# Optimization experiments

Measured on AMD Instinct MI355X. Metric: run time of the kernel, lower is better.

## Reference

```python
import jax, jax.numpy as jnp
import numpy as np
from jax import lax


def _conv(x, w, b, pad):
    # x: [B,C,H,W], w: [O,I,kh,kw]
    y = lax.conv_general_dilated(x, w, (1, 1), [(pad, pad), (pad, pad)],
                                 dimension_numbers=('NCHW', 'OIHW', 'NCHW'))
    return y + b[None, :, None, None]


def _maxpool2(x):
    return lax.reduce_window(x, -jnp.inf, lax.max, (1, 1, 2, 2), (1, 1, 2, 2), 'VALID')


def setup_inputs() -> dict:
    key = jax.random.key(0)
    ks = jax.random.split(key, 6)
    N, T, R, D = 8, 64, 9, 512
    x = jax.random.normal(ks[0], (N, T, R, D), dtype=jnp.float32)
    x = x / jnp.linalg.norm(x, axis=-1, keepdims=True)  # ViSiL features are L2-normalized
    w1 = jax.random.normal(ks[1], (32, 1, 3, 3), dtype=jnp.float32) * 0.05
    w2 = jax.random.normal(ks[2], (64, 32, 3, 3), dtype=jnp.float32) * 0.05
    w3 = jax.random.normal(ks[3], (128, 64, 3, 3), dtype=jnp.float32) * 0.05
    w4 = jax.random.normal(ks[4], (1, 128, 1, 1), dtype=jnp.float32) * 0.05
    return {
        'x': x,
        'w1': w1, 'b1': jnp.zeros((32,), jnp.float32),
        'w2': w2, 'b2': jnp.zeros((64,), jnp.float32),
        'w3': w3, 'b3': jnp.zeros((128,), jnp.float32),
        'w4': w4, 'b4': jnp.zeros((1,), jnp.float32),
    }


def reference(x, w1, b1, w2, b2, w3, b3, w4, b4):
    N, T, R, D = x.shape
    # frame-to-frame similarity: region correlation volume + chamfer (max over p, mean over o)
    sim = jnp.einsum('aiok,bjpk->aiopjb', x, x)        # [a,i,o,p,j,b]
    sim = jnp.mean(jnp.max(sim, axis=3), axis=2)        # [a,i,j,b]
    sim = jnp.transpose(sim, (0, 3, 1, 2)).reshape(N * N, 1, T, T)  # '(a b) () i j'
    # VideoComparator CNN head (ZeroPad2d(1) + valid 3x3 conv == 'same' 3x3 conv)
    h = jax.nn.relu(_conv(sim, w1, b1, 1))
    h = _maxpool2(h)
    h = jax.nn.relu(_conv(h, w2, b2, 1))
    h = _maxpool2(h)
    h = jax.nn.relu(_conv(h, w3, b3, 1))
    h = _conv(h, w4, b4, 0)                              # [N*N, 1, T/4, T/4]
    # SimilarityRegularizationLoss(min_val=-1, max_val=1)
    loss = jnp.sum(jax.nn.relu(-(h + 1.0))) + jnp.sum(jax.nn.relu(h - 1.0))
    # Hardtanh, rescale to [0,1], then video-to-video chamfer
    s = jnp.clip(h, -1.0, 1.0) / 2.0 + 0.5
    s = jnp.mean(jnp.max(s, axis=3), axis=2)             # [N*N, 1]
    return s.reshape(N, N), loss
```

## Files before the change

### kernel.cpp

```cpp
#include <hip/hip_runtime.h>

typedef unsigned short u16;
typedef unsigned int u32;
typedef __bf16 bf16x8 __attribute__((ext_vector_type(8)));
typedef u16 u16x8 __attribute__((ext_vector_type(8)));
typedef float f32x4 __attribute__((ext_vector_type(4)));

__device__ __forceinline__ u16 f2bf(float f) {
  u32 u = __float_as_uint(f);
  u32 r = (u + 0x7FFFu + ((u >> 16) & 1u)) >> 16;
  return (u16)r;
}

__device__ __forceinline__ void gload16(const void* g, void* l) {
  typedef __attribute__((address_space(1))) const void gvoid;
  typedef __attribute__((address_space(3))) void lvoid;
  __builtin_amdgcn_global_load_lds((gvoid*)g, (lvoid*)l, 16, 0, 0);
}

__global__ void k_cast(const float* __restrict__ x, u16* __restrict__ A) {
  int t = blockIdx.x * 256 + threadIdx.x;
  const float4* xp = (const float4*)x + (size_t)t * 2;
  float4 v0 = xp[0], v1 = xp[1];
  u16x8 r;
  r[0] = f2bf(v0.x); r[1] = f2bf(v0.y); r[2] = f2bf(v0.z); r[3] = f2bf(v0.w);
  r[4] = f2bf(v1.x); r[5] = f2bf(v1.y); r[6] = f2bf(v1.z); r[7] = f2bf(v1.w);
  *(u16x8*)(A + (size_t)t * 8) = r;
}

__global__ __launch_bounds__(256) void k_gemm_smax(const u16* __restrict__ A,
                                                   float* __restrict__ Smax) {
  __shared__ char smem[53248];
  u16* As = (u16*)smem;
  u16* Bs = (u16*)(smem + 16384);
  const int rb = blockIdx.x, cb = blockIdx.y;
  const int rowBase = rb * 128, colBase = cb * 288;
  const int tid = threadIdx.x, wave = tid >> 6, lane = tid & 63;
  const int lr = lane >> 3, lc = lane & 7;
  const int lrow = lane & 15, lk = lane >> 4;
  const int xr = lrow & 7;
  const int wr = (wave & 1) * 64, wc = (wave >> 1) * 144;

  f32x4 acc[4][9];
#pragma unroll
  for (int rt = 0; rt < 4; ++rt)
#pragma unroll
    for (int ct = 0; ct < 9; ++ct) { f32x4 z = {0.f, 0.f, 0.f, 0.f}; acc[rt][ct] = z; }

  for (int k0 = 0; k0 < 512; k0 += 64) {
    __syncthreads();
#pragma unroll
    for (int ii = 0; ii < 4; ++ii) {
      int r0 = wave * 32 + ii * 8;
      gload16(A + (size_t)(rowBase + r0 + lr) * 512 + k0 + ((lc ^ lr) * 8),
              As + r0 * 64);
    }
#pragma unroll
    for (int jj = 0; jj < 9; ++jj) {
      int c0 = wave * 72 + jj * 8;
      gload16(A + (size_t)(colBase + c0 + lr) * 512 + k0 + ((lc ^ lr) * 8),
              Bs + c0 * 64);
    }
    __syncthreads();
#pragma unroll
    for (int s = 0; s < 2; ++s) {
      bf16x8 af[4], bf[9];
#pragma unroll
      for (int rt = 0; rt < 4; ++rt)
        af[rt] = *(const bf16x8*)(As + (wr + rt * 16 + lrow) * 64 +
                                  ((u32)(s * 4 + lk) ^ xr) * 8);
#pragma unroll
      for (int ct = 0; ct < 9; ++ct)
        bf[ct] = *(const bf16x8*)(Bs + (wc + ct * 16 + lrow) * 64 +
                                  ((u32)(s * 4 + lk) ^ xr) * 8);
#pragma unroll
      for (int rt = 0; rt < 4; ++rt)
#pragma unroll
        for (int ct = 0; ct < 9; ++ct)
          acc[rt][ct] = __builtin_amdgcn_mfma_f32_16x16x32_bf16(af[rt], bf[ct],
                                                                acc[rt][ct], 0, 0, 0);
    }
  }

  float* epi = (float*)smem + wave * 2368;
  const int w2 = wave >> 1;
#pragma unroll
  for (int rt = 0; rt < 4; ++rt) {
    __syncthreads();
#pragma unroll
    for (int ct = 0; ct < 9; ++ct)
#pragma unroll
      for (int r = 0; r < 4; ++r)
        epi[(lk * 4 + r) * 148 + ct * 16 + lrow] = acc[rt][ct][r];
    __syncthreads();
#pragma unroll
    for (int q = 0; q < 4; ++q) {
      int o = lane + 64 * q;
      int row = o >> 4, g = o & 15;
      const float* p = epi + row * 148 + g * 9;
      float m = p[0];
#pragma unroll
      for (int t = 1; t < 9; ++t) m = fmaxf(m, p[t]);
      Smax[(size_t)(rowBase + wr + rt * 16 + row) * 512 + cb * 32 + w2 * 16 + g] = m;
    }
  }
}

__global__ void k_reduce_o(const float* __restrict__ Smax, float* __restrict__ sim) {
  int idx = blockIdx.x * 256 + threadIdx.x;
  int j = idx & 63, i = (idx >> 6) & 63, b = (idx >> 12) & 7, a = idx >> 15;
  const float* p = Smax + (size_t)((a * 64 + i) * 9) * 512 + b * 64 + j;
  float s = p[0];
#pragma unroll
  for (int o = 1; o < 9; ++o) s += p[o * 512];
  sim[idx] = s * (1.f / 9.f);
}

__global__ void k_wpack(const float* __restrict__ w2, const float* __restrict__ w3,
                        u16* __restrict__ p2, u16* __restrict__ p3) {
  int i = blockIdx.x * 256 + threadIdx.x;
  if (i < 18432) {
    int t = i >> 11, oc = (i >> 5) & 63, ic = i & 31;
    p2[i] = f2bf(w2[(oc * 32 + ic) * 9 + t]);
  }
  {
    int t = i >> 13, oc = (i >> 6) & 127, ic = i & 63;
    p3[i] = f2bf(w3[(oc * 64 + ic) * 9 + t]);
  }
}

__global__ __launch_bounds__(256) void k_conv1pool(const float* __restrict__ sim,
                                                   const float* __restrict__ w1,
                                                   const float* __restrict__ b1,
                                                   u16* __restrict__ h1) {
  __shared__ float tin[4096];
  const int pair = blockIdx.x, ocg = blockIdx.y, tid = threadIdx.x;
  const float4* src = (const float4*)(sim + (size_t)pair * 4096);
  for (int i = tid; i < 1024; i += 256) ((float4*)tin)[i] = src[i];
  __syncthreads();
  float wv[8][9], bs[8];
#pragma unroll
  for (int o = 0; o < 8; ++o) {
#pragma unroll
    for (int q = 0; q < 9; ++q) wv[o][q] = w1[(ocg * 8 + o) * 9 + q];
    bs[o] = b1[ocg * 8 + o];
  }
  for (int pp = tid; pp < 1024; pp += 256) {
    int py = pp >> 5, px = pp & 31;
    float m[8];
#pragma unroll
    for (int o = 0; o < 8; ++o) m[o] = 0.f;
#pragma unroll
    for (int dy = 0; dy < 2; ++dy)
#pragma unroll
      for (int dx = 0; dx < 2; ++dx) {
        float s[8];
#pragma unroll
        for (int o = 0; o < 8; ++o) s[o] = bs[o];
        int yy = py * 2 + dy, xx0 = px * 2 + dx;
#pragma unroll
        for (int ky = 0; ky < 3; ++ky) {
          int y = yy + ky - 1;
          if ((unsigned)y < 64u) {
#pragma unroll
            for (int kx = 0; kx < 3; ++kx) {
              int x = xx0 + kx - 1;
              if ((unsigned)x < 64u) {
                float v = tin[y * 64 + x];
#pragma unroll
                for (int o = 0; o < 8; ++o) s[o] += wv[o][ky * 3 + kx] * v;
              }
            }
          }
        }
#pragma unroll
        for (int o = 0; o < 8; ++o) m[o] = fmaxf(m[o], fmaxf(s[o], 0.f));
      }
    u16x8 r;
#pragma unroll
    for (int o = 0; o < 8; ++o) r[o] = f2bf(m[o]);
    *(u16x8*)&h1[(((size_t)pair * 32 + py) * 32 + px) * 32 + ocg * 8] = r;
  }
}

__global__ __launch_bounds__(256) void k_conv2pool(const u16* __restrict__ h1,
                                                   const u16* __restrict__ wp2,
                                                   const float* __restrict__ b2,
                                                   u16* __restrict__ h2) {
  __shared__ u16 tile[18 * 34 * 40];
  const int pair = blockIdx.x, yh = blockIdx.y, tid = threadIdx.x;
  const int wave = tid >> 6, lane = tid & 63, l15 = lane & 15, quad = lane >> 4;
  u16x8 z8 = {0, 0, 0, 0, 0, 0, 0, 0};
  for (int i = tid; i < 3060; i += 256) ((u16x8*)tile)[i] = z8;
  __syncthreads();
  for (int f = tid; f < 1152; f += 256) {
    int i = f >> 6, rem = f & 63, px = rem >> 1, half = rem & 1;
    int gr = yh * 16 - 1 + i;
    if ((unsigned)gr < 32u)
      *(u16x8*)&tile[(i * 34 + 1 + px) * 40 + half * 16] =
          *(const u16x8*)&h1[(((size_t)pair * 32 + gr) * 32 + px) * 32 + half * 16];
  }
  __syncthreads();

  f32x4 acc[8][4];
#pragma unroll
  for (int m = 0; m < 8; ++m)
#pragma unroll
    for (int n = 0; n < 4; ++n) { f32x4 z = {0.f, 0.f, 0.f, 0.f}; acc[m][n] = z; }

  for (int t = 0; t < 9; ++t) {
    int ky = t / 3, kx = t % 3;
    bf16x8 wf[4];
#pragma unroll
    for (int nt = 0; nt < 4; ++nt)
      wf[nt] = *(const bf16x8*)&wp2[((t * 64 + nt * 16 + l15) << 5) + quad * 8];
#pragma unroll
    for (int rr = 0; rr < 4; ++rr)
#pragma unroll
      for (int xh = 0; xh < 2; ++xh) {
        int lr = wave * 4 + rr;
        bf16x8 af = *(const bf16x8*)&tile[((lr + ky) * 34 + xh * 16 + l15 + kx) * 40 +
                                          quad * 8];
#pragma unroll
        for (int nt = 0; nt < 4; ++nt)
          acc[rr * 2 + xh][nt] =
              __builtin_amdgcn_mfma_f32_16x16x32_bf16(af, wf[nt], acc[rr * 2 + xh][nt],
                                                      0, 0, 0);
      }
  }

  float bv[4];
#pragma unroll
  for (int nt = 0; nt < 4; ++nt) bv[nt] = b2[nt * 16 + l15];
#pragma unroll
  for (int rp = 0; rp < 2; ++rp)
#pragma unroll
    for (int xh = 0; xh < 2; ++xh) {
      int py = yh * 8 + wave * 2 + rp;
      int px0 = xh * 8 + quad * 2;
#pragma unroll
      for (int nt = 0; nt < 4; ++nt) {
        f32x4 va = acc[(rp * 2) * 2 + xh][nt], vb = acc[(rp * 2 + 1) * 2 + xh][nt];
        float p0 = fmaxf(fmaxf(fmaxf(va[0], va[1]), fmaxf(vb[0], vb[1])) + bv[nt], 0.f);
        float p1 = fmaxf(fmaxf(fmaxf(va[2], va[3]), fmaxf(vb[2], vb[3])) + bv[nt], 0.f);
        size_t base = (((size_t)pair * 16 + py) * 16 + px0) * 64 + nt * 16 + l15;
        h2[base] = f2bf(p0);
        h2[base + 64] = f2bf(p1);
      }
    }
}

__global__ __launch_bounds__(256) void k_conv3(const u16* __restrict__ h2,
                                               const u16* __restrict__ wp3,
                                               const float* __restrict__ b3,
                                               float* __restrict__ h3) {
  __shared__ u16 tile[18 * 18 * 72];
  const int pair = blockIdx.x, oh = blockIdx.y, tid = threadIdx.x;
  const int wave = tid >> 6, lane = tid & 63, l15 = lane & 15, quad = lane >> 4;
  u16x8 z8 = {0, 0, 0, 0, 0, 0, 0, 0};
  for (int i = tid; i < 2916; i += 256) ((u16x8*)tile)[i] = z8;
  __syncthreads();
  for (int f = tid; f < 2048; f += 256) {
    int row = f >> 7, rem = f & 127, px = rem >> 3, seg = rem & 7;
    *(u16x8*)&tile[((row + 1) * 18 + px + 1) * 72 + seg * 8] =
        *(const u16x8*)&h2[(((size_t)pair * 16 + row) * 16 + px) * 64 + seg * 8];
  }
  __syncthreads();

  f32x4 acc[4][4];
#pragma unroll
  for (int m = 0; m < 4; ++m)
#pragma unroll
    for (int n = 0; n < 4; ++n) { f32x4 z = {0.f, 0.f, 0.f, 0.f}; acc[m][n] = z; }

  for (int t = 0; t < 9; ++t) {
    int ky = t / 3, kx = t % 3;
#pragma unroll
    for (int s = 0; s < 2; ++s) {
      bf16x8 wf[4];
#pragma unroll
      for (int nt = 0; nt < 4; ++nt)
        wf[nt] = *(const bf16x8*)&wp3[((t * 128 + oh * 64 + nt * 16 + l15) << 6) +
                                      s * 32 + quad * 8];
#pragma unroll
      for (int yt = 0; yt < 4; ++yt) {
        int y = wave * 4 + yt;
        bf16x8 af = *(const bf16x8*)&tile[((y + ky) * 18 + l15 + kx) * 72 + s * 32 +
                                          quad * 8];
#pragma unroll
        for (int nt = 0; nt < 4; ++nt)
          acc[yt][nt] = __builtin_amdgcn_mfma_f32_16x16x32_bf16(af, wf[nt],
                                                                acc[yt][nt], 0, 0, 0);
      }
    }
  }

  float bv[4];
#pragma unroll
  for (int nt = 0; nt < 4; ++nt) bv[nt] = b3[oh * 64 + nt * 16 + l15];
#pragma unroll
  for (int yt = 0; yt < 4; ++yt)
#pragma unroll
    for (int nt = 0; nt < 4; ++nt)
#pragma unroll
      for (int r = 0; r < 4; ++r) {
        int px = (wave * 4 + yt) * 16 + quad * 4 + r;
        h3[((size_t)pair * 256 + px) * 128 + oh * 64 + nt * 16 + l15] =
            fmaxf(acc[yt][nt][r] + bv[nt], 0.f);
      }
}

__global__ void k_zero(float* __restrict__ out) {
  if (threadIdx.x < 65) out[threadIdx.x] = 0.f;
}

__global__ __launch_bounds__(256) void k_conv4(const float* __restrict__ h3,
                                               const float* __restrict__ w4,
                                               const float* __restrict__ b4,
                                               float* __restrict__ out) {
  __shared__ float ws4[128];
  __shared__ float rowmax[16];
  __shared__ float lsum[4];
  const int pair = blockIdx.x, tid = threadIdx.x;
  if (tid < 128) ws4[tid] = w4[tid];
  __syncthreads();
  float h = b4[0];
  const float4* p = (const float4*)(h3 + ((size_t)pair * 256 + tid) * 128);
#pragma unroll 8
  for (int i = 0; i < 32; ++i) {
    float4 v = p[i];
    h += v.x * ws4[i * 4] + v.y * ws4[i * 4 + 1] + v.z * ws4[i * 4 + 2] +
         v.w * ws4[i * 4 + 3];
  }
  float loss = fmaxf(-(h + 1.f), 0.f) + fmaxf(h - 1.f, 0.f);
  float sc = fminf(fmaxf(h, -1.f), 1.f) * 0.5f + 0.5f;
#pragma unroll
  for (int off = 8; off >= 1; off >>= 1) sc = fmaxf(sc, __shfl_xor(sc, off, 16));
#pragma unroll
  for (int off = 32; off >= 1; off >>= 1) loss += __shfl_xor(loss, off, 64);
  if ((tid & 15) == 0) rowmax[tid >> 4] = sc;
  if ((tid & 63) == 0) lsum[tid >> 6] = loss;
  __syncthreads();
  if (tid == 0) {
    float mean = 0.f;
#pragma unroll
    for (int i = 0; i < 16; ++i) mean += rowmax[i];
    out[pair] = mean * (1.f / 16.f);
    atomicAdd(out + 64, lsum[0] + lsum[1] + lsum[2] + lsum[3]);
  }
}

extern "C" void kernel_launch(void* const* d_in, const int* in_sizes, int n_in,
                              void* d_out, int out_size, void* d_ws, size_t ws_size,
                              hipStream_t stream) {
  (void)in_sizes; (void)n_in; (void)out_size; (void)ws_size;
  const float* x  = (const float*)d_in[0];
  const float* w1 = (const float*)d_in[1];
  const float* b1 = (const float*)d_in[2];
  const float* w2 = (const float*)d_in[3];
  const float* b2 = (const float*)d_in[4];
  const float* w3 = (const float*)d_in[5];
  const float* b3 = (const float*)d_in[6];
  const float* w4 = (const float*)d_in[7];
  const float* b4 = (const float*)d_in[8];
  float* out = (float*)d_out;

  char* ws = (char*)d_ws;
  u16*   Abf  = (u16*)ws;
  float* Smax = (float*)(ws + 4718592);
  float* sim  = (float*)(ws + 14155776);
  u16*   h1   = (u16*)(ws + 15204352);
  u16*   h2   = (u16*)(ws + 19398656);
  float* h3   = (float*)(ws + 21495808);
  u16*   wp2  = (u16*)(ws + 29884416);
  u16*   wp3  = (u16*)(ws + 29921280);

  k_cast<<<1152, 256, 0, stream>>>(x, Abf);
  k_gemm_smax<<<dim3(36, 16), 256, 0, stream>>>(Abf, Smax);
  k_reduce_o<<<1024, 256, 0, stream>>>(Smax, sim);
  k_wpack<<<288, 256, 0, stream>>>(w2, w3, wp2, wp3);
  k_conv1pool<<<dim3(64, 4), 256, 0, stream>>>(sim, w1, b1, h1);
  k_conv2pool<<<dim3(64, 2), 256, 0, stream>>>(h1, wp2, b2, h2);
  k_conv3<<<dim3(64, 2), 256, 0, stream>>>(h2, wp3, b3, h3);
  k_zero<<<1, 128, 0, stream>>>(out);
  k_conv4<<<64, 256, 0, stream>>>(h3, w4, b4, out);
}
```

Before: 177.5 us.

## Replace LDS-staged GEMM with single-wave blocks loading operands directly from global

The correlation GEMM no longer stages A and B tiles in shared memory through global_load_lds with block-wide barriers. Each block is now one wave computing a 64x144 tile, and it reads its MFMA operand fragments straight from global memory every 32-wide k step. This drops the LDS traffic and synchronisation and raises the block count. In exchange, the tiles shared between waves are no longer reused through LDS, so global/L2 traffic grows and the strided 16-byte loads may expose memory latency.

```diff
diff --git a/kernel.cpp b/kernel.cpp
--- a/kernel.cpp
+++ b/kernel.cpp
@@ -10,12 +10,6 @@
   u32 u = __float_as_uint(f);
   u32 r = (u + 0x7FFFu + ((u >> 16) & 1u)) >> 16;
   return (u16)r;
-}
-
-__device__ __forceinline__ void gload16(const void* g, void* l) {
-  typedef __attribute__((address_space(1))) const void gvoid;
-  typedef __attribute__((address_space(3))) void lvoid;
-  __builtin_amdgcn_global_load_lds((gvoid*)g, (lvoid*)l, 16, 0, 0);
 }
 
 __global__ void k_cast(const float* __restrict__ x, u16* __restrict__ A) {
@@ -28,18 +22,16 @@
   *(u16x8*)(A + (size_t)t * 8) = r;
 }
 
-__global__ __launch_bounds__(256) void k_gemm_smax(const u16* __restrict__ A,
-                                                   float* __restrict__ Smax) {
-  __shared__ char smem[53248];
-  u16* As = (u16*)smem;
-  u16* Bs = (u16*)(smem + 16384);
+__global__ __launch_bounds__(64, 2) void k_gemm_smax(const u16* __restrict__ A,
+                                                     float* __restrict__ Smax) {
+  __shared__ float epi[16 * 148];
   const int rb = blockIdx.x, cb = blockIdx.y;
-  const int rowBase = rb * 128, colBase = cb * 288;
-  const int tid = threadIdx.x, wave = tid >> 6, lane = tid & 63;
-  const int lr = lane >> 3, lc = lane & 7;
+  const int rowBase = rb * 64, colBase = cb * 144;
+  const int lane = threadIdx.x;
   const int lrow = lane & 15, lk = lane >> 4;
-  const int xr = lrow & 7;
-  const int wr = (wave & 1) * 64, wc = (wave >> 1) * 144;
+
+  const u16* Ap = A + (size_t)(rowBase + lrow) * 512 + lk * 8;
+  const u16* Bp = A + (size_t)(colBase + lrow) * 512 + lk * 8;
 
   f32x4 acc[4][9];
 #pragma unroll
@@ -47,43 +39,23 @@
 #pragma unroll
     for (int ct = 0; ct < 9; ++ct) { f32x4 z = {0.f, 0.f, 0.f, 0.f}; acc[rt][ct] = z; }
 
-  for (int k0 = 0; k0 < 512; k0 += 64) {
-    __syncthreads();
-#pragma unroll
-    for (int ii = 0; ii < 4; ++ii) {
-      int r0 = wave * 32 + ii * 8;
-      gload16(A + (size_t)(rowBase + r0 + lr) * 512 + k0 + ((lc ^ lr) * 8),
-              As + r0 * 64);
-    }
-#pragma unroll
-    for (int jj = 0; jj < 9; ++jj) {
-      int c0 = wave * 72 + jj * 8;
-      gload16(A + (size_t)(colBase + c0 + lr) * 512 + k0 + ((lc ^ lr) * 8),
-              Bs + c0 * 64);
-    }
-    __syncthreads();
-#pragma unroll
-    for (int s = 0; s < 2; ++s) {
-      bf16x8 af[4], bf[9];
-#pragma unroll
-      for (int rt = 0; rt < 4; ++rt)
-        af[rt] = *(const bf16x8*)(As + (wr + rt * 16 + lrow) * 64 +
-                                  ((u32)(s * 4 + lk) ^ xr) * 8);
+#pragma unroll 1
+  for (int k0 = 0; k0 < 512; k0 += 32) {
+    bf16x8 af[4], bf[9];
+#pragma unroll
+    for (int rt = 0; rt < 4; ++rt)
+      af[rt] = *(const bf16x8*)(Ap + (size_t)rt * 16 * 512 + k0);
+#pragma unroll
+    for (int ct = 0; ct < 9; ++ct)
+      bf[ct] = *(const bf16x8*)(Bp + (size_t)ct * 16 * 512 + k0);
+#pragma unroll
+    for (int rt = 0; rt < 4; ++rt)
 #pragma unroll
       for (int ct = 0; ct < 9; ++ct)
-        bf[ct] = *(const bf16x8*)(Bs + (wc + ct * 16 + lrow) * 64 +
-                                  ((u32)(s * 4 + lk) ^ xr) * 8);
-#pragma unroll
-      for (int rt = 0; rt < 4; ++rt)
-#pragma unroll
-        for (int ct = 0; ct < 9; ++ct)
-          acc[rt][ct] = __builtin_amdgcn_mfma_f32_16x16x32_bf16(af[rt], bf[ct],
-                                                                acc[rt][ct], 0, 0, 0);
-    }
-  }
-
-  float* epi = (float*)smem + wave * 2368;
-  const int w2 = wave >> 1;
+        acc[rt][ct] = __builtin_amdgcn_mfma_f32_16x16x32_bf16(af[rt], bf[ct],
+                                                              acc[rt][ct], 0, 0, 0);
+  }
+
 #pragma unroll
   for (int rt = 0; rt < 4; ++rt) {
     __syncthreads();
@@ -101,7 +73,7 @@
       float m = p[0];
 #pragma unroll
       for (int t = 1; t < 9; ++t) m = fmaxf(m, p[t]);
-      Smax[(size_t)(rowBase + wr + rt * 16 + row) * 512 + cb * 32 + w2 * 16 + g] = m;
+      Smax[(size_t)(rowBase + rt * 16 + row) * 512 + cb * 16 + g] = m;
     }
   }
 }
@@ -376,7 +348,7 @@
   u16*   wp3  = (u16*)(ws + 29921280);
 
   k_cast<<<1152, 256, 0, stream>>>(x, Abf);
-  k_gemm_smax<<<dim3(36, 16), 256, 0, stream>>>(Abf, Smax);
+  k_gemm_smax<<<dim3(72, 32), 64, 0, stream>>>(Abf, Smax);
   k_reduce_o<<<1024, 256, 0, stream>>>(Smax, sim);
   k_wpack<<<288, 256, 0, stream>>>(w2, w3, wp2, wp3);
   k_conv1pool<<<dim3(64, 4), 256, 0, stream>>>(sim, w1, b1, h1);
```

Measured after the change: 193.9 us. +9.3%, slower.

## Exploit Gram symmetry: compute upper-triangle GEMM tiles and emit both max directions

Applied to the files above, without the earlier changes.

The region Gram matrix x·xᵀ is symmetric, so the GEMM now uses square 128x128 tiles and launches only blocks with rb<=cb. Each block reduces its tile along both rows and columns to produce the p-max for both orientations. Groups of nine that straddle tile boundaries go to a side buffer Sx, and the consumer merges them. The o-mean reduction is folded into conv1pool, which now handles all four channel groups per block, and the output zeroing moves into k_wpack, dropping two launches. In exchange the epilogue is more complex with partial-group handling, about half the launched blocks exit immediately, and conv1 has fewer blocks.

```diff
diff --git a/kernel.cpp b/kernel.cpp
--- a/kernel.cpp
+++ b/kernel.cpp
@@ -29,23 +29,26 @@
 }
 
 __global__ __launch_bounds__(256) void k_gemm_smax(const u16* __restrict__ A,
-                                                   float* __restrict__ Smax) {
-  __shared__ char smem[53248];
+                                                   float* __restrict__ Smax,
+                                                   float* __restrict__ Sx) {
+  __shared__ char smem[33536];
+  const int rb = blockIdx.x, cb = blockIdx.y;
+  if (rb > cb) return;
   u16* As = (u16*)smem;
   u16* Bs = (u16*)(smem + 16384);
-  const int rb = blockIdx.x, cb = blockIdx.y;
-  const int rowBase = rb * 128, colBase = cb * 288;
+  float* slab = (float*)smem;
+  const int rowBase = rb * 128, colBase = cb * 128;
   const int tid = threadIdx.x, wave = tid >> 6, lane = tid & 63;
   const int lr = lane >> 3, lc = lane & 7;
   const int lrow = lane & 15, lk = lane >> 4;
   const int xr = lrow & 7;
-  const int wr = (wave & 1) * 64, wc = (wave >> 1) * 144;
-
-  f32x4 acc[4][9];
+  const int wr = (wave & 1) * 64, wc = (wave >> 1) * 64;
+
+  f32x4 acc[4][4];
 #pragma unroll
   for (int rt = 0; rt < 4; ++rt)
 #pragma unroll
-    for (int ct = 0; ct < 9; ++ct) { f32x4 z = {0.f, 0.f, 0.f, 0.f}; acc[rt][ct] = z; }
+    for (int ct = 0; ct < 4; ++ct) { f32x4 z = {0.f, 0.f, 0.f, 0.f}; acc[rt][ct] = z; }
 
   for (int k0 = 0; k0 < 512; k0 += 64) {
     __syncthreads();
@@ -54,71 +57,92 @@
       int r0 = wave * 32 + ii * 8;
       gload16(A + (size_t)(rowBase + r0 + lr) * 512 + k0 + ((lc ^ lr) * 8),
               As + r0 * 64);
-    }
-#pragma unroll
-    for (int jj = 0; jj < 9; ++jj) {
-      int c0 = wave * 72 + jj * 8;
-      gload16(A + (size_t)(colBase + c0 + lr) * 512 + k0 + ((lc ^ lr) * 8),
-              Bs + c0 * 64);
+      gload16(A + (size_t)(colBase + r0 + lr) * 512 + k0 + ((lc ^ lr) * 8),
+              Bs + r0 * 64);
     }
     __syncthreads();
 #pragma unroll
     for (int s = 0; s < 2; ++s) {
-      bf16x8 af[4], bf[9];
+      bf16x8 af[4], bf[4];
 #pragma unroll
       for (int rt = 0; rt < 4; ++rt)
         af[rt] = *(const bf16x8*)(As + (wr + rt * 16 + lrow) * 64 +
                                   ((u32)(s * 4 + lk) ^ xr) * 8);
 #pragma unroll
-      for (int ct = 0; ct < 9; ++ct)
+      for (int ct = 0; ct < 4; ++ct)
         bf[ct] = *(const bf16x8*)(Bs + (wc + ct * 16 + lrow) * 64 +
                                   ((u32)(s * 4 + lk) ^ xr) * 8);
 #pragma unroll
       for (int rt = 0; rt < 4; ++rt)
 #pragma unroll
-        for (int ct = 0; ct < 9; ++ct)
+        for (int ct = 0; ct < 4; ++ct)
           acc[rt][ct] = __builtin_amdgcn_mfma_f32_16x16x32_bf16(af[rt], bf[ct],
                                                                 acc[rt][ct], 0, 0, 0);
     }
   }
 
-  float* epi = (float*)smem + wave * 2368;
-  const int w2 = wave >> 1;
-#pragma unroll
-  for (int rt = 0; rt < 4; ++rt) {
+  const int g0c = colBase / 9, offc = colBase % 9;
+  const int g0r = rowBase / 9, offr = rowBase % 9;
+  const int nph = (rb == cb) ? 2 : 4;
+  for (int ph = 0; ph < nph; ++ph) {
     __syncthreads();
-#pragma unroll
-    for (int ct = 0; ct < 9; ++ct)
-#pragma unroll
-      for (int r = 0; r < 4; ++r)
-        epi[(lk * 4 + r) * 148 + ct * 16 + lrow] = acc[rt][ct][r];
+    if (ph < 2) {
+      if ((wave & 1) == ph) {
+#pragma unroll
+        for (int rt = 0; rt < 4; ++rt)
+#pragma unroll
+          for (int ct = 0; ct < 4; ++ct)
+#pragma unroll
+            for (int r = 0; r < 4; ++r)
+              slab[(rt * 16 + lk * 4 + r) * 129 + wc + ct * 16 + lrow] = acc[rt][ct][r];
+      }
+    } else {
+      if ((wave >> 1) == ph - 2) {
+#pragma unroll
+        for (int rt = 0; rt < 4; ++rt)
+#pragma unroll
+          for (int ct = 0; ct < 4; ++ct)
+#pragma unroll
+            for (int r = 0; r < 4; ++r)
+              slab[(ct * 16 + lrow) * 129 + wr + rt * 16 + lk * 4 + r] = acc[rt][ct][r];
+      }
+    }
     __syncthreads();
-#pragma unroll
-    for (int q = 0; q < 4; ++q) {
-      int o = lane + 64 * q;
-      int row = o >> 4, g = o & 15;
-      const float* p = epi + row * 148 + g * 9;
-      float m = p[0];
-#pragma unroll
-      for (int t = 1; t < 9; ++t) m = fmaxf(m, p[t]);
-      Smax[(size_t)(rowBase + wr + rt * 16 + row) * 512 + cb * 32 + w2 * 16 + g] = m;
-    }
-  }
-}
-
-__global__ void k_reduce_o(const float* __restrict__ Smax, float* __restrict__ sim) {
-  int idx = blockIdx.x * 256 + threadIdx.x;
-  int j = idx & 63, i = (idx >> 6) & 63, b = (idx >> 12) & 7, a = idx >> 15;
-  const float* p = Smax + (size_t)((a * 64 + i) * 9) * 512 + b * 64 + j;
-  float s = p[0];
-#pragma unroll
-  for (int o = 1; o < 9; ++o) s += p[o * 512];
-  sim[idx] = s * (1.f / 9.f);
+    for (int it = tid; it < 1024; it += 256) {
+      int line = it >> 4, s = it & 15;
+      float m = -3.0e38f;
+      if (ph < 2) {
+        int g = g0c + s;
+        int cs = 9 * g - colBase, ce = cs + 9;
+        cs = cs < 0 ? 0 : cs;
+        ce = ce > 128 ? 128 : ce;
+        if (cs >= ce) continue;
+        const float* p = slab + line * 129;
+        for (int c = cs; c < ce; ++c) m = fmaxf(m, p[c]);
+        int r = rowBase + ph * 64 + line;
+        if (s == 0 && offc != 0) Sx[(size_t)r * 36 + (cb - 1)] = m;
+        else Smax[(size_t)r * 512 + g] = m;
+      } else {
+        int g = g0r + s;
+        int rs = 9 * g - rowBase, re = rs + 9;
+        rs = rs < 0 ? 0 : rs;
+        re = re > 128 ? 128 : re;
+        if (rs >= re) continue;
+        const float* p = slab + line * 129;
+        for (int r2 = rs; r2 < re; ++r2) m = fmaxf(m, p[r2]);
+        int cgl = colBase + (ph - 2) * 64 + line;
+        if (s == 0 && offr != 0) Sx[(size_t)cgl * 36 + (rb - 1)] = m;
+        else Smax[(size_t)cgl * 512 + g] = m;
+      }
+    }
+  }
 }
 
 __global__ void k_wpack(const float* __restrict__ w2, const float* __restrict__ w3,
-                        u16* __restrict__ p2, u16* __restrict__ p3) {
+                        u16* __restrict__ p2, u16* __restrict__ p3,
+                        float* __restrict__ out) {
   int i = blockIdx.x * 256 + threadIdx.x;
+  if (blockIdx.x == 0 && threadIdx.x < 65) out[threadIdx.x] = 0.f;
   if (i < 18432) {
     int t = i >> 11, oc = (i >> 5) & 63, ic = i & 31;
     p2[i] = f2bf(w2[(oc * 32 + ic) * 9 + t]);
@@ -129,57 +153,76 @@
   }
 }
 
-__global__ __launch_bounds__(256) void k_conv1pool(const float* __restrict__ sim,
+__global__ __launch_bounds__(256) void k_conv1pool(const float* __restrict__ Smax,
+                                                   const float* __restrict__ Sx,
                                                    const float* __restrict__ w1,
                                                    const float* __restrict__ b1,
                                                    u16* __restrict__ h1) {
   __shared__ float tin[4096];
-  const int pair = blockIdx.x, ocg = blockIdx.y, tid = threadIdx.x;
-  const float4* src = (const float4*)(sim + (size_t)pair * 4096);
-  for (int i = tid; i < 1024; i += 256) ((float4*)tin)[i] = src[i];
-  __syncthreads();
-  float wv[8][9], bs[8];
-#pragma unroll
-  for (int o = 0; o < 8; ++o) {
-#pragma unroll
-    for (int q = 0; q < 9; ++q) wv[o][q] = w1[(ocg * 8 + o) * 9 + q];
-    bs[o] = b1[ocg * 8 + o];
-  }
-  for (int pp = tid; pp < 1024; pp += 256) {
-    int py = pp >> 5, px = pp & 31;
-    float m[8];
-#pragma unroll
-    for (int o = 0; o < 8; ++o) m[o] = 0.f;
-#pragma unroll
-    for (int dy = 0; dy < 2; ++dy)
-#pragma unroll
-      for (int dx = 0; dx < 2; ++dx) {
-        float s[8];
-#pragma unroll
-        for (int o = 0; o < 8; ++o) s[o] = bs[o];
-        int yy = py * 2 + dy, xx0 = px * 2 + dx;
-#pragma unroll
-        for (int ky = 0; ky < 3; ++ky) {
-          int y = yy + ky - 1;
-          if ((unsigned)y < 64u) {
-#pragma unroll
-            for (int kx = 0; kx < 3; ++kx) {
-              int x = xx0 + kx - 1;
-              if ((unsigned)x < 64u) {
-                float v = tin[y * 64 + x];
-#pragma unroll
-                for (int o = 0; o < 8; ++o) s[o] += wv[o][ky * 3 + kx] * v;
+  const int pair = blockIdx.x, tid = threadIdx.x;
+  const int a = pair >> 3, b = pair & 7;
+  for (int it = tid; it < 4096; it += 256) {
+    int i = it >> 6, j = it & 63;
+    int g = b * 64 + j;
+    int t9 = 9 * g;
+    int k = (t9 + 8) >> 7;
+    bool part = ((u32)(128 * k - t9 - 1) < 8u);
+    float s = 0.f;
+    const float* p = Smax + (size_t)(a * 576 + i * 9) * 512 + g;
+    const float* q = Sx + (size_t)(a * 576 + i * 9) * 36 + (k - 1);
+#pragma unroll
+    for (int o = 0; o < 9; ++o) {
+      float v = p[o * 512];
+      if (part) v = fmaxf(v, q[o * 36]);
+      s += v;
+    }
+    tin[it] = s * (1.f / 9.f);
+  }
+  __syncthreads();
+  for (int ocg = 0; ocg < 4; ++ocg) {
+    float wv[8][9], bs[8];
+#pragma unroll
+    for (int o = 0; o < 8; ++o) {
+#pragma unroll
+      for (int q = 0; q < 9; ++q) wv[o][q] = w1[(ocg * 8 + o) * 9 + q];
+      bs[o] = b1[ocg * 8 + o];
+    }
+    for (int pp = tid; pp < 1024; pp += 256) {
+      int py = pp >> 5, px = pp & 31;
+      float m[8];
+#pragma unroll
+      for (int o = 0; o < 8; ++o) m[o] = 0.f;
+#pragma unroll
+      for (int dy = 0; dy < 2; ++dy)
+#pragma unroll
+        for (int dx = 0; dx < 2; ++dx) {
+          float s[8];
+#pragma unroll
+          for (int o = 0; o < 8; ++o) s[o] = bs[o];
+          int yy = py * 2 + dy, xx0 = px * 2 + dx;
+#pragma unroll
+          for (int ky = 0; ky < 3; ++ky) {
+            int y = yy + ky - 1;
+            if ((unsigned)y < 64u) {
+#pragma unroll
+              for (int kx = 0; kx < 3; ++kx) {
+                int x = xx0 + kx - 1;
+                if ((unsigned)x < 64u) {
+                  float v = tin[y * 64 + x];
+#pragma unroll
+                  for (int o = 0; o < 8; ++o) s[o] += wv[o][ky * 3 + kx] * v;
+                }
               }
             }
           }
+#pragma unroll
+          for (int o = 0; o < 8; ++o) m[o] = fmaxf(m[o], fmaxf(s[o], 0.f));
         }
-#pragma unroll
-        for (int o = 0; o < 8; ++o) m[o] = fmaxf(m[o], fmaxf(s[o], 0.f));
-      }
-    u16x8 r;
-#pragma unroll
-    for (int o = 0; o < 8; ++o) r[o] = f2bf(m[o]);
-    *(u16x8*)&h1[(((size_t)pair * 32 + py) * 32 + px) * 32 + ocg * 8] = r;
+      u16x8 r;
+#pragma unroll
+      for (int o = 0; o < 8; ++o) r[o] = f2bf(m[o]);
+      *(u16x8*)&h1[(((size_t)pair * 32 + py) * 32 + px) * 32 + ocg * 8] = r;
+    }
   }
 }
 
@@ -308,10 +351,6 @@
         h3[((size_t)pair * 256 + px) * 128 + oh * 64 + nt * 16 + l15] =
             fmaxf(acc[yt][nt][r] + bv[nt], 0.f);
       }
-}
-
-__global__ void k_zero(float* __restrict__ out) {
-  if (threadIdx.x < 65) out[threadIdx.x] = 0.f;
 }
 
 __global__ __launch_bounds__(256) void k_conv4(const float* __restrict__ h3,
@@ -368,20 +407,18 @@
   char* ws = (char*)d_ws;
   u16*   Abf  = (u16*)ws;
   float* Smax = (float*)(ws + 4718592);
-  float* sim  = (float*)(ws + 14155776);
-  u16*   h1   = (u16*)(ws + 15204352);
-  u16*   h2   = (u16*)(ws + 19398656);
-  float* h3   = (float*)(ws + 21495808);
-  u16*   wp2  = (u16*)(ws + 29884416);
-  u16*   wp3  = (u16*)(ws + 29921280);
+  float* Sx   = (float*)(ws + 14155776);
+  u16*   h1   = (u16*)(ws + 14819328);
+  u16*   h2   = (u16*)(ws + 19013632);
+  float* h3   = (float*)(ws + 21110784);
+  u16*   wp2  = (u16*)(ws + 29499392);
+  u16*   wp3  = (u16*)(ws + 29536256);
 
   k_cast<<<1152, 256, 0, stream>>>(x, Abf);
-  k_gemm_smax<<<dim3(36, 16), 256, 0, stream>>>(Abf, Smax);
-  k_reduce_o<<<1024, 256, 0, stream>>>(Smax, sim);
-  k_wpack<<<288, 256, 0, stream>>>(w2, w3, wp2, wp3);
-  k_conv1pool<<<dim3(64, 4), 256, 0, stream>>>(sim, w1, b1, h1);
+  k_gemm_smax<<<dim3(36, 36), 256, 0, stream>>>(Abf, Smax, Sx);
+  k_wpack<<<288, 256, 0, stream>>>(w2, w3, wp2, wp3, out);
+  k_conv1pool<<<64, 256, 0, stream>>>(Smax, Sx, w1, b1, h1);
   k_conv2pool<<<dim3(64, 2), 256, 0, stream>>>(h1, wp2, b2, h2);
   k_conv3<<<dim3(64, 2), 256, 0, stream>>>(h2, wp3, b3, h3);
-  k_zero<<<1, 128, 0, stream>>>(out);
   k_conv4<<<64, 256, 0, stream>>>(h3, w4, b4, out);
 }
```

Result: slower. 225.8 us (+27.2%).
